# Optimization experiments

Hardware: AMD Instinct MI355X
Metric: run time of the kernel (lower is better)

The kernel has to match this reference:

```python
import jax, jax.numpy as jnp
import numpy as np

N_NODES = 100000


def setup_inputs() -> dict:
    key = jax.random.key(0)
    k1, k2, k3, k4, k5 = jax.random.split(key, 5)
    n_edges = 1600000
    d_in, d_out = 128, 128
    input_features = jax.random.normal(k1, (N_NODES, d_in), dtype=jnp.float32)
    weight = jax.random.normal(k2, (d_in, d_out), dtype=jnp.float32) * (1.0 / np.sqrt(d_out))
    edge_vals = jax.random.uniform(k3, (n_edges,), dtype=jnp.float32)
    edge_src = jax.random.randint(k4, (n_edges,), 0, N_NODES, dtype=jnp.int32)
    edge_dst = jax.random.randint(k5, (n_edges,), 0, N_NODES, dtype=jnp.int32)
    return {
        "input_features": input_features,
        "weight": weight,
        "edge_vals": edge_vals,
        "edge_src": edge_src,
        "edge_dst": edge_dst,
    }


def reference(input_features, weight, edge_vals, edge_src, edge_dst):
    neg_slope = 0.0
    # dense transform: support = X @ W  -> [N, d_out]
    support = input_features @ weight
    # sparse SpMM: out[dst] += val * support[src]  (COO adjacency)
    msgs = edge_vals[:, None] * support[edge_src]  # [E, d_out]
    output = jax.ops.segment_sum(msgs, edge_dst, num_segments=N_NODES)
    # leaky_relu with negative_slope = neg_slope (0 -> relu)
    return jnp.where(output >= 0, output, neg_slope * output)
```

## Files before the change

kernel.cpp:

```cpp
#include <hip/hip_runtime.h>
#include <hip/hip_bf16.h>


#define D 128
#define NB_SHIFT 7
#define BNODES 128
#define MAXB 1024
#define CAPB 2560
#define RPT 10
#define XSTR 144

using bf16x8 = __attribute__((ext_vector_type(8))) short;
using f32x4  = __attribute__((ext_vector_type(4))) float;

__device__ inline unsigned short f2bf(float f) {
    unsigned u = __float_as_uint(f);
    u += 0x7fffu + ((u >> 16) & 1u);
    return (unsigned short)(u >> 16);
}
__device__ inline float bflo(unsigned w) { return __uint_as_float(w << 16); }
__device__ inline float bfhi(unsigned w) { return __uint_as_float(w & 0xffff0000u); }

__global__ __launch_bounds__(256) void wtrans(const float* __restrict__ W,
                                              unsigned short* __restrict__ WT,
                                              int* cursor, int nb) {
    const int t = threadIdx.x, b = blockIdx.x;
    const int n  = (b << 4) | (t & 15);
    const int k0 = (t >> 4) << 3;
#pragma unroll
    for (int k = k0; k < k0 + 8; ++k)
        WT[n * D + k] = f2bf(W[k * D + n]);
    if (b == 0)
        for (int i = t; i < nb; i += 256) cursor[i] = 0;
}

__global__ __launch_bounds__(256) void gemm_mfma(const float* __restrict__ X,
                                                 const unsigned short* __restrict__ WT,
                                                 unsigned short* __restrict__ S,
                                                 int nRows) {
    __shared__ unsigned short Xl[64 * XSTR];
    __shared__ unsigned short Wl[128 * XSTR];

    const int t = threadIdx.x;
    const int row0 = blockIdx.x * 64;

    const uint4* WT4 = (const uint4*)WT;
    uint4* Wl4 = (uint4*)Wl;
#pragma unroll
    for (int i = t; i < 2048; i += 256) {
        int n = i >> 4, kc8 = i & 15;
        Wl4[n * (XSTR / 8) + kc8] = WT4[i];
    }

    const float4* X4 = (const float4*)X;
    ushort4* Xl4 = (ushort4*)Xl;
#pragma unroll
    for (int i = t; i < 2048; i += 256) {
        int r = i >> 5, c = i & 31;
        int gr = row0 + r;
        float4 v = make_float4(0.f, 0.f, 0.f, 0.f);
        if (gr < nRows) v = X4[(size_t)gr * 32 + c];
        ushort4 p;
        p.x = f2bf(v.x); p.y = f2bf(v.y); p.z = f2bf(v.z); p.w = f2bf(v.w);
        Xl4[r * (XSTR / 4) + c] = p;
    }
    __syncthreads();

    const int wv = t >> 6, lane = t & 63;
    const int m = lane & 15, quad = lane >> 4;
    const int m0 = wv << 4;

    f32x4 acc[8];
    f32x4 z = {0.f, 0.f, 0.f, 0.f};
#pragma unroll
    for (int nt = 0; nt < 8; ++nt) acc[nt] = z;

#pragma unroll
    for (int kc = 0; kc < 4; ++kc) {
        bf16x8 a = *(const bf16x8*)(Xl + (m0 + m) * XSTR + kc * 32 + quad * 8);
#pragma unroll
        for (int nt = 0; nt < 8; ++nt) {
            bf16x8 b = *(const bf16x8*)(Wl + (nt * 16 + m) * XSTR + kc * 32 + quad * 8);
            acc[nt] = __builtin_amdgcn_mfma_f32_16x16x32_bf16(a, b, acc[nt], 0, 0, 0);
        }
    }

#pragma unroll
    for (int nt = 0; nt < 8; ++nt) {
#pragma unroll
        for (int r = 0; r < 4; ++r) {
            int gr = row0 + m0 + quad * 4 + r;
            if (gr < nRows) S[(size_t)gr * D + nt * 16 + m] = f2bf(acc[nt][r]);
        }
    }
}

__global__ __launch_bounds__(256) void fill2(const int* __restrict__ src,
                                             const int* __restrict__ dst,
                                             const float* __restrict__ vals,
                                             int* gcursor, int2* __restrict__ epk,
                                             int E, int nb) {
    __shared__ int h[MAXB];
    __shared__ int cur[MAXB];
    const int t = threadIdx.x;
    for (int i = t; i < nb; i += 256) h[i] = 0;
    __syncthreads();

    int chunk = (E + gridDim.x - 1) / gridDim.x;
    chunk = (chunk + 3) & ~3;
    const int s0 = min(E, (int)blockIdx.x * chunk);
    const int s1 = min(E, s0 + chunk);
    const int vend = s0 + (((s1 - s0) >> 10) << 10);

    int e = s0 + (t << 2);
    for (; e + 1028 <= vend; e += 2048) {
        int4 da = *(const int4*)(dst + e);
        int4 db = *(const int4*)(dst + e + 1024);
        atomicAdd(&h[da.x >> NB_SHIFT], 1);
        atomicAdd(&h[da.y >> NB_SHIFT], 1);
        atomicAdd(&h[da.z >> NB_SHIFT], 1);
        atomicAdd(&h[da.w >> NB_SHIFT], 1);
        atomicAdd(&h[db.x >> NB_SHIFT], 1);
        atomicAdd(&h[db.y >> NB_SHIFT], 1);
        atomicAdd(&h[db.z >> NB_SHIFT], 1);
        atomicAdd(&h[db.w >> NB_SHIFT], 1);
    }
    for (; e + 4 <= vend; e += 1024) {
        int4 d = *(const int4*)(dst + e);
        atomicAdd(&h[d.x >> NB_SHIFT], 1);
        atomicAdd(&h[d.y >> NB_SHIFT], 1);
        atomicAdd(&h[d.z >> NB_SHIFT], 1);
        atomicAdd(&h[d.w >> NB_SHIFT], 1);
    }
    for (e = vend + t; e < s1; e += 256) atomicAdd(&h[dst[e] >> NB_SHIFT], 1);
    __syncthreads();

    for (int i = t; i < nb; i += 256) {
        int c = h[i];
        cur[i] = c ? (i * CAPB + atomicAdd(&gcursor[i], c)) : 0;
    }
    __syncthreads();

    e = s0 + (t << 2);
    for (; e + 1028 <= vend; e += 2048) {
        int4   da = *(const int4*)(dst + e);
        int4   sa = *(const int4*)(src + e);
        float4 va = *(const float4*)(vals + e);
        int4   db = *(const int4*)(dst + e + 1024);
        int4   sb = *(const int4*)(src + e + 1024);
        float4 vb = *(const float4*)(vals + e + 1024);
        int p0 = atomicAdd(&cur[da.x >> NB_SHIFT], 1);
        int p1 = atomicAdd(&cur[da.y >> NB_SHIFT], 1);
        int p2 = atomicAdd(&cur[da.z >> NB_SHIFT], 1);
        int p3 = atomicAdd(&cur[da.w >> NB_SHIFT], 1);
        epk[p0] = make_int2(sa.x | ((da.x & 127) << 20), __float_as_int(va.x));
        epk[p1] = make_int2(sa.y | ((da.y & 127) << 20), __float_as_int(va.y));
        epk[p2] = make_int2(sa.z | ((da.z & 127) << 20), __float_as_int(va.z));
        epk[p3] = make_int2(sa.w | ((da.w & 127) << 20), __float_as_int(va.w));
        int q0 = atomicAdd(&cur[db.x >> NB_SHIFT], 1);
        int q1 = atomicAdd(&cur[db.y >> NB_SHIFT], 1);
        int q2 = atomicAdd(&cur[db.z >> NB_SHIFT], 1);
        int q3 = atomicAdd(&cur[db.w >> NB_SHIFT], 1);
        epk[q0] = make_int2(sb.x | ((db.x & 127) << 20), __float_as_int(vb.x));
        epk[q1] = make_int2(sb.y | ((db.y & 127) << 20), __float_as_int(vb.y));
        epk[q2] = make_int2(sb.z | ((db.z & 127) << 20), __float_as_int(vb.z));
        epk[q3] = make_int2(sb.w | ((db.w & 127) << 20), __float_as_int(vb.w));
    }
    for (; e + 4 <= vend; e += 1024) {
        int4   d = *(const int4*)(dst + e);
        int4   s = *(const int4*)(src + e);
        float4 v = *(const float4*)(vals + e);
        int p0 = atomicAdd(&cur[d.x >> NB_SHIFT], 1);
        int p1 = atomicAdd(&cur[d.y >> NB_SHIFT], 1);
        int p2 = atomicAdd(&cur[d.z >> NB_SHIFT], 1);
        int p3 = atomicAdd(&cur[d.w >> NB_SHIFT], 1);
        epk[p0] = make_int2(s.x | ((d.x & 127) << 20), __float_as_int(v.x));
        epk[p1] = make_int2(s.y | ((d.y & 127) << 20), __float_as_int(v.y));
        epk[p2] = make_int2(s.z | ((d.z & 127) << 20), __float_as_int(v.z));
        epk[p3] = make_int2(s.w | ((d.w & 127) << 20), __float_as_int(v.w));
    }
    for (e = vend + t; e < s1; e += 256) {
        int d = dst[e];
        int pos = atomicAdd(&cur[d >> NB_SHIFT], 1);
        epk[pos] = make_int2(src[e] | ((d & 127) << 20), __float_as_int(vals[e]));
    }
}

__global__ __launch_bounds__(256, 4) void bucket_gather(const unsigned short* __restrict__ support,
                                                        const int* __restrict__ gcursor,
                                                        const int2* __restrict__ epk,
                                                        float* __restrict__ out, int N) {
    __shared__ int2 se[CAPB];
    __shared__ int  hist[BNODES];
    __shared__ int  rows[BNODES];
    __shared__ int  cur[BNODES];

    const int t   = threadIdx.x;
    const int b   = blockIdx.x;
    const int cnt = min(gcursor[b], CAPB);
    const int beg = b * CAPB;

    if (t < BNODES) hist[t] = 0;
    __syncthreads();

    int2 r[RPT];
#pragma unroll
    for (int i = 0; i < RPT; ++i) {
        int idx = t + (i << 8);
        if (idx < cnt) r[i] = epk[beg + idx];
    }
#pragma unroll
    for (int i = 0; i < RPT; ++i) {
        int idx = t + (i << 8);
        if (idx < cnt) atomicAdd(&hist[(r[i].x >> 20) & 127], 1);
    }
    __syncthreads();

    if (t < BNODES) rows[t] = hist[t];
    __syncthreads();
#pragma unroll
    for (int off = 1; off < BNODES; off <<= 1) {
        int v = 0;
        if (t < BNODES && t >= off) v = rows[t - off];
        __syncthreads();
        if (t < BNODES && t >= off) rows[t] += v;
        __syncthreads();
    }
    if (t < BNODES) cur[t] = rows[t] - hist[t];
    __syncthreads();

#pragma unroll
    for (int i = 0; i < RPT; ++i) {
        int idx = t + (i << 8);
        if (idx < cnt) {
            int pos = atomicAdd(&cur[(r[i].x >> 20) & 127], 1);
            se[pos] = r[i];
        }
    }
    __syncthreads();

    const int g = t >> 4, lane = t & 15;
    const int node0 = b << NB_SHIFT;
    const uint4* S4 = (const uint4*)support;
    float4* o4 = (float4*)out;

    for (int nn = g; nn < BNODES; nn += 16) {
        const int send = rows[nn];
        const int sbeg = send - hist[nn];

        float a[8];
#pragma unroll
        for (int k = 0; k < 8; ++k) a[k] = 0.f;

        int j = sbeg;
        for (; j + 3 < send; j += 4) {
            int2 e0 = se[j], e1 = se[j + 1], e2 = se[j + 2], e3 = se[j + 3];
            uint4 m0 = S4[(size_t)(e0.x & 0xFFFFF) * 16 + lane];
            uint4 m1 = S4[(size_t)(e1.x & 0xFFFFF) * 16 + lane];
            uint4 m2 = S4[(size_t)(e2.x & 0xFFFFF) * 16 + lane];
            uint4 m3 = S4[(size_t)(e3.x & 0xFFFFF) * 16 + lane];
            float v0 = __int_as_float(e0.y), v1 = __int_as_float(e1.y);
            float v2 = __int_as_float(e2.y), v3 = __int_as_float(e3.y);
            a[0] = fmaf(v0, bflo(m0.x), a[0]); a[1] = fmaf(v0, bfhi(m0.x), a[1]);
            a[2] = fmaf(v0, bflo(m0.y), a[2]); a[3] = fmaf(v0, bfhi(m0.y), a[3]);
            a[4] = fmaf(v0, bflo(m0.z), a[4]); a[5] = fmaf(v0, bfhi(m0.z), a[5]);
            a[6] = fmaf(v0, bflo(m0.w), a[6]); a[7] = fmaf(v0, bfhi(m0.w), a[7]);
            a[0] = fmaf(v1, bflo(m1.x), a[0]); a[1] = fmaf(v1, bfhi(m1.x), a[1]);
            a[2] = fmaf(v1, bflo(m1.y), a[2]); a[3] = fmaf(v1, bfhi(m1.y), a[3]);
            a[4] = fmaf(v1, bflo(m1.z), a[4]); a[5] = fmaf(v1, bfhi(m1.z), a[5]);
            a[6] = fmaf(v1, bflo(m1.w), a[6]); a[7] = fmaf(v1, bfhi(m1.w), a[7]);
            a[0] = fmaf(v2, bflo(m2.x), a[0]); a[1] = fmaf(v2, bfhi(m2.x), a[1]);
            a[2] = fmaf(v2, bflo(m2.y), a[2]); a[3] = fmaf(v2, bfhi(m2.y), a[3]);
            a[4] = fmaf(v2, bflo(m2.z), a[4]); a[5] = fmaf(v2, bfhi(m2.z), a[5]);
            a[6] = fmaf(v2, bflo(m2.w), a[6]); a[7] = fmaf(v2, bfhi(m2.w), a[7]);
            a[0] = fmaf(v3, bflo(m3.x), a[0]); a[1] = fmaf(v3, bfhi(m3.x), a[1]);
            a[2] = fmaf(v3, bflo(m3.y), a[2]); a[3] = fmaf(v3, bfhi(m3.y), a[3]);
            a[4] = fmaf(v3, bflo(m3.z), a[4]); a[5] = fmaf(v3, bfhi(m3.z), a[5]);
            a[6] = fmaf(v3, bflo(m3.w), a[6]); a[7] = fmaf(v3, bfhi(m3.w), a[7]);
        }
        for (; j < send; ++j) {
            int2 e0 = se[j];
            uint4 m0 = S4[(size_t)(e0.x & 0xFFFFF) * 16 + lane];
            float v0 = __int_as_float(e0.y);
            a[0] = fmaf(v0, bflo(m0.x), a[0]); a[1] = fmaf(v0, bfhi(m0.x), a[1]);
            a[2] = fmaf(v0, bflo(m0.y), a[2]); a[3] = fmaf(v0, bfhi(m0.y), a[3]);
            a[4] = fmaf(v0, bflo(m0.z), a[4]); a[5] = fmaf(v0, bfhi(m0.z), a[5]);
            a[6] = fmaf(v0, bflo(m0.w), a[6]); a[7] = fmaf(v0, bfhi(m0.w), a[7]);
        }

        const int gn = node0 + nn;
        if (gn < N) {
            size_t base = (size_t)gn * 32 + 2 * lane;
            float4 lo = make_float4(fmaxf(a[0], 0.f), fmaxf(a[1], 0.f),
                                    fmaxf(a[2], 0.f), fmaxf(a[3], 0.f));
            float4 hi = make_float4(fmaxf(a[4], 0.f), fmaxf(a[5], 0.f),
                                    fmaxf(a[6], 0.f), fmaxf(a[7], 0.f));
            o4[base]     = lo;
            o4[base + 1] = hi;
        }
    }
}

extern "C" void kernel_launch(void* const* d_in, const int* in_sizes, int n_in,
                              void* d_out, int out_size, void* d_ws, size_t ws_size,
                              hipStream_t stream) {
    const float* X    = (const float*)d_in[0];
    const float* W    = (const float*)d_in[1];
    const float* vals = (const float*)d_in[2];
    const int*   src  = (const int*)d_in[3];
    const int*   dst  = (const int*)d_in[4];
    float*       out  = (float*)d_out;

    const int N  = in_sizes[0] / D;
    const int E  = in_sizes[2];
    const int nb = (N + BNODES - 1) / BNODES;

    size_t off = 0;
    auto take = [&](size_t bytes) {
        size_t p = off;
        off = (off + bytes + 255) & ~(size_t)255;
        return p;
    };
    char* ws = (char*)d_ws;
    size_t o_support = take((size_t)N * D * sizeof(unsigned short));
    size_t o_wt      = take((size_t)D * D * sizeof(unsigned short));
    size_t o_cursor  = take((size_t)nb * sizeof(int));
    size_t o_epk     = take(((size_t)nb * CAPB + 1024) * sizeof(int2));
    (void)ws_size;

    unsigned short* support = (unsigned short*)(ws + o_support);
    unsigned short* WT      = (unsigned short*)(ws + o_wt);
    int*  cursor = (int*)(ws + o_cursor);
    int2* epk    = (int2*)(ws + o_epk);

    wtrans<<<8, 256, 0, stream>>>(W, WT, cursor, nb);

    gemm_mfma<<<(N + 63) / 64, 256, 0, stream>>>(X, WT, support, N);

    fill2<<<256, 256, 0, stream>>>(src, dst, vals, cursor, epk, E, nb);

    bucket_gather<<<nb, 256, 0, stream>>>(support, cursor, epk, out, N);
}
```

Measured before the change: 220.4 us.

## Halve destination bucket size, widen fill blocks, and raise gather occupancy

Destination buckets shrink from 128 to 64 nodes, so there are twice as many gather blocks, each with a smaller shared edge buffer. The gather kernel's launch bound is raised to target 8 blocks per CU, and its node loop is unrolled. The fill kernel now runs 1024-thread blocks with a simpler single vectorized loop. The GEMM LDS row stride also changes, and bucket capacity is lowered to 1408 (mean load is about 1024 edges), which risks silently dropping edges in an overfull bucket.

```diff
diff --git a/kernel.cpp b/kernel.cpp
--- a/kernel.cpp
+++ b/kernel.cpp
@@ -3,12 +3,12 @@
 
 
 #define D 128
-#define NB_SHIFT 7
-#define BNODES 128
-#define MAXB 1024
-#define CAPB 2560
-#define RPT 10
-#define XSTR 144
+#define NB_SHIFT 6
+#define BNODES 64
+#define MAXB 2048
+#define CAPB 1408
+#define RPT 6
+#define XSTR 136
 
 using bf16x8 = __attribute__((ext_vector_type(8))) short;
 using f32x4  = __attribute__((ext_vector_type(4))) float;
@@ -95,78 +95,42 @@
     }
 }
 
-__global__ __launch_bounds__(256) void fill2(const int* __restrict__ src,
-                                             const int* __restrict__ dst,
-                                             const float* __restrict__ vals,
-                                             int* gcursor, int2* __restrict__ epk,
-                                             int E, int nb) {
+__global__ __launch_bounds__(1024, 4) void fill2(const int* __restrict__ src,
+                                                 const int* __restrict__ dst,
+                                                 const float* __restrict__ vals,
+                                                 int* gcursor, int2* __restrict__ epk,
+                                                 int E, int nb) {
     __shared__ int h[MAXB];
     __shared__ int cur[MAXB];
     const int t = threadIdx.x;
-    for (int i = t; i < nb; i += 256) h[i] = 0;
+    for (int i = t; i < nb; i += 1024) h[i] = 0;
     __syncthreads();
 
     int chunk = (E + gridDim.x - 1) / gridDim.x;
     chunk = (chunk + 3) & ~3;
     const int s0 = min(E, (int)blockIdx.x * chunk);
     const int s1 = min(E, s0 + chunk);
-    const int vend = s0 + (((s1 - s0) >> 10) << 10);
+    const int vend = s0 + ((s1 - s0) & ~3);
 
     int e = s0 + (t << 2);
-    for (; e + 1028 <= vend; e += 2048) {
-        int4 da = *(const int4*)(dst + e);
-        int4 db = *(const int4*)(dst + e + 1024);
-        atomicAdd(&h[da.x >> NB_SHIFT], 1);
-        atomicAdd(&h[da.y >> NB_SHIFT], 1);
-        atomicAdd(&h[da.z >> NB_SHIFT], 1);
-        atomicAdd(&h[da.w >> NB_SHIFT], 1);
-        atomicAdd(&h[db.x >> NB_SHIFT], 1);
-        atomicAdd(&h[db.y >> NB_SHIFT], 1);
-        atomicAdd(&h[db.z >> NB_SHIFT], 1);
-        atomicAdd(&h[db.w >> NB_SHIFT], 1);
-    }
-    for (; e + 4 <= vend; e += 1024) {
+    for (; e + 4 <= vend; e += 4096) {
         int4 d = *(const int4*)(dst + e);
         atomicAdd(&h[d.x >> NB_SHIFT], 1);
         atomicAdd(&h[d.y >> NB_SHIFT], 1);
         atomicAdd(&h[d.z >> NB_SHIFT], 1);
         atomicAdd(&h[d.w >> NB_SHIFT], 1);
     }
-    for (e = vend + t; e < s1; e += 256) atomicAdd(&h[dst[e] >> NB_SHIFT], 1);
-    __syncthreads();
-
-    for (int i = t; i < nb; i += 256) {
+    for (e = vend + t; e < s1; e += 1024) atomicAdd(&h[dst[e] >> NB_SHIFT], 1);
+    __syncthreads();
+
+    for (int i = t; i < nb; i += 1024) {
         int c = h[i];
         cur[i] = c ? (i * CAPB + atomicAdd(&gcursor[i], c)) : 0;
     }
     __syncthreads();
 
     e = s0 + (t << 2);
-    for (; e + 1028 <= vend; e += 2048) {
-        int4   da = *(const int4*)(dst + e);
-        int4   sa = *(const int4*)(src + e);
-        float4 va = *(const float4*)(vals + e);
-        int4   db = *(const int4*)(dst + e + 1024);
-        int4   sb = *(const int4*)(src + e + 1024);
-        float4 vb = *(const float4*)(vals + e + 1024);
-        int p0 = atomicAdd(&cur[da.x >> NB_SHIFT], 1);
-        int p1 = atomicAdd(&cur[da.y >> NB_SHIFT], 1);
-        int p2 = atomicAdd(&cur[da.z >> NB_SHIFT], 1);
-        int p3 = atomicAdd(&cur[da.w >> NB_SHIFT], 1);
-        epk[p0] = make_int2(sa.x | ((da.x & 127) << 20), __float_as_int(va.x));
-        epk[p1] = make_int2(sa.y | ((da.y & 127) << 20), __float_as_int(va.y));
-        epk[p2] = make_int2(sa.z | ((da.z & 127) << 20), __float_as_int(va.z));
-        epk[p3] = make_int2(sa.w | ((da.w & 127) << 20), __float_as_int(va.w));
-        int q0 = atomicAdd(&cur[db.x >> NB_SHIFT], 1);
-        int q1 = atomicAdd(&cur[db.y >> NB_SHIFT], 1);
-        int q2 = atomicAdd(&cur[db.z >> NB_SHIFT], 1);
-        int q3 = atomicAdd(&cur[db.w >> NB_SHIFT], 1);
-        epk[q0] = make_int2(sb.x | ((db.x & 127) << 20), __float_as_int(vb.x));
-        epk[q1] = make_int2(sb.y | ((db.y & 127) << 20), __float_as_int(vb.y));
-        epk[q2] = make_int2(sb.z | ((db.z & 127) << 20), __float_as_int(vb.z));
-        epk[q3] = make_int2(sb.w | ((db.w & 127) << 20), __float_as_int(vb.w));
-    }
-    for (; e + 4 <= vend; e += 1024) {
+    for (; e + 4 <= vend; e += 4096) {
         int4   d = *(const int4*)(dst + e);
         int4   s = *(const int4*)(src + e);
         float4 v = *(const float4*)(vals + e);
@@ -174,19 +138,19 @@
         int p1 = atomicAdd(&cur[d.y >> NB_SHIFT], 1);
         int p2 = atomicAdd(&cur[d.z >> NB_SHIFT], 1);
         int p3 = atomicAdd(&cur[d.w >> NB_SHIFT], 1);
-        epk[p0] = make_int2(s.x | ((d.x & 127) << 20), __float_as_int(v.x));
-        epk[p1] = make_int2(s.y | ((d.y & 127) << 20), __float_as_int(v.y));
-        epk[p2] = make_int2(s.z | ((d.z & 127) << 20), __float_as_int(v.z));
-        epk[p3] = make_int2(s.w | ((d.w & 127) << 20), __float_as_int(v.w));
-    }
-    for (e = vend + t; e < s1; e += 256) {
+        epk[p0] = make_int2(s.x | ((d.x & (BNODES - 1)) << 20), __float_as_int(v.x));
+        epk[p1] = make_int2(s.y | ((d.y & (BNODES - 1)) << 20), __float_as_int(v.y));
+        epk[p2] = make_int2(s.z | ((d.z & (BNODES - 1)) << 20), __float_as_int(v.z));
+        epk[p3] = make_int2(s.w | ((d.w & (BNODES - 1)) << 20), __float_as_int(v.w));
+    }
+    for (e = vend + t; e < s1; e += 1024) {
         int d = dst[e];
         int pos = atomicAdd(&cur[d >> NB_SHIFT], 1);
-        epk[pos] = make_int2(src[e] | ((d & 127) << 20), __float_as_int(vals[e]));
-    }
-}
-
-__global__ __launch_bounds__(256, 4) void bucket_gather(const unsigned short* __restrict__ support,
+        epk[pos] = make_int2(src[e] | ((d & (BNODES - 1)) << 20), __float_as_int(vals[e]));
+    }
+}
+
+__global__ __launch_bounds__(256, 8) void bucket_gather(const unsigned short* __restrict__ support,
                                                         const int* __restrict__ gcursor,
                                                         const int2* __restrict__ epk,
                                                         float* __restrict__ out, int N) {
@@ -212,7 +176,7 @@
 #pragma unroll
     for (int i = 0; i < RPT; ++i) {
         int idx = t + (i << 8);
-        if (idx < cnt) atomicAdd(&hist[(r[i].x >> 20) & 127], 1);
+        if (idx < cnt) atomicAdd(&hist[(r[i].x >> 20) & (BNODES - 1)], 1);
     }
     __syncthreads();
 
@@ -233,7 +197,7 @@
     for (int i = 0; i < RPT; ++i) {
         int idx = t + (i << 8);
         if (idx < cnt) {
-            int pos = atomicAdd(&cur[(r[i].x >> 20) & 127], 1);
+            int pos = atomicAdd(&cur[(r[i].x >> 20) & (BNODES - 1)], 1);
             se[pos] = r[i];
         }
     }
@@ -244,6 +208,7 @@
     const uint4* S4 = (const uint4*)support;
     float4* o4 = (float4*)out;
 
+#pragma unroll
     for (int nn = g; nn < BNODES; nn += 16) {
         const int send = rows[nn];
         const int sbeg = send - hist[nn];
@@ -337,7 +302,7 @@
 
     gemm_mfma<<<(N + 63) / 64, 256, 0, stream>>>(X, WT, support, N);
 
-    fill2<<<256, 256, 0, stream>>>(src, dst, vals, cursor, epk, E, nb);
+    fill2<<<256, 1024, 0, stream>>>(src, dst, vals, cursor, epk, E, nb);
 
     bucket_gather<<<nb, 256, 0, stream>>>(support, cursor, epk, out, N);
 }
```

After: 218.5 us. No clear change (-0.9%).
